# Performance work log

Hardware: AMD Instinct MI355X
Metric: run time of the kernel (lower is better)

Reference implementation:

```python
import jax, jax.numpy as jnp
import numpy as np

N = 20000        # nodes
E = 640000       # edges (avg degree 32)
IN, H1, H2 = 512, 256, 128

def setup_inputs() -> dict:
    key = jax.random.key(0)
    k_feat, k_ew, k_src, k_dst, k_w1, k_w2 = jax.random.split(key, 6)
    return {
        "features": jax.random.normal(k_feat, (N, IN), jnp.float32),
        "edge_weight": jax.random.uniform(k_ew, (E,), jnp.float32),
        "src": jax.random.randint(k_src, (E,), 0, N),
        "dst": jax.random.randint(k_dst, (E,), 0, N),
        # learned params (GraphConv weight uses xavier-style init; bias zeros)
        "W1": jax.random.normal(k_w1, (IN, H1), jnp.float32) / np.float32(np.sqrt(IN)),
        "b1": jnp.zeros((H1,), jnp.float32),
        "W2": jax.random.normal(k_w2, (H1, H2), jnp.float32) / np.float32(np.sqrt(H1)),
        "b2": jnp.zeros((H2,), jnp.float32),
    }

def reference(features, edge_weight, src, dst, W1, b1, W2, b2):
    seg = lambda v, idx: jax.ops.segment_sum(v, idx, num_segments=N)

    # --- EdgeWeightNorm(norm='both'):
    # w_e / sqrt(out_wsum(src_e) * in_wsum(dst_e))
    out_wsum = seg(edge_weight, src)           # weighted out-degree  [N]
    in_wsum = seg(edge_weight, dst)            # weighted in-degree   [N]
    nw = edge_weight * jax.lax.rsqrt(out_wsum[src]) * jax.lax.rsqrt(in_wsum[dst])  # [E]

    # --- GraphConv layer 1: norm='none', edge_weight=nw, relu
    # in_feats > out_feats -> transform first, then weighted aggregation
    h = features @ W1                          # [N, H1]
    h = seg(h[src] * nw[:, None], dst) + b1    # SpMM: sum_e nw_e * h[src_e] at dst
    h = jax.nn.relu(h)

    # --- GraphConv layer 2: norm='both' (plain degrees, clamped min 1), identity act
    ones_e = jnp.ones((E,), h.dtype)
    out_deg = jnp.maximum(seg(ones_e, src), 1.0)   # out-degrees [N]
    in_deg = jnp.maximum(seg(ones_e, dst), 1.0)    # in-degrees  [N]
    h = h * jax.lax.rsqrt(out_deg)[:, None]        # src-side norm
    h = h @ W2                                     # [N, H2] (in > out -> W first)
    h = seg(h[src], dst)                           # unweighted sum aggregation
    h = h * jax.lax.rsqrt(in_deg)[:, None] + b2    # dst-side norm + bias
    return h
```

## Files before the change

kernel.cpp:

```cpp
#include <hip/hip_runtime.h>
#include <hip/hip_bf16.h>
#include <hip/hip_fp16.h>
#include <stdint.h>

#define IN_F 512
#define H1_F 256
#define H2_F 128
#define MPAD 20096
#define NN   20000
#define NPAIR 10000
#define BH   128
#define CAP  128

typedef __attribute__((ext_vector_type(8))) _Float16 half8;
typedef __attribute__((ext_vector_type(4))) float f32x4;
typedef __attribute__((ext_vector_type(4))) uint32_t u32x4;

__device__ inline __half2 h2cast(uint32_t v) { return __builtin_bit_cast(__half2, v); }
__device__ inline uint32_t h2bits(__half2 v) { return __builtin_bit_cast(uint32_t, v); }

__device__ inline void gld_lds16(const uint32_t* g, uint32_t* l) {
    __builtin_amdgcn_global_load_lds((const __attribute__((address_space(1))) uint32_t*)g,
                                     (__attribute__((address_space(3))) uint32_t*)l,
                                     16, 0, 0);
}

__global__ __launch_bounds__(512) void build_and_pack(
        const int* __restrict__ dst, const int* __restrict__ src,
        const float* __restrict__ ew,
        uint32_t* __restrict__ Pd, uint32_t* __restrict__ Ps, int E, int CH,
        const float4* __restrict__ X, ushort4* __restrict__ P, int n4,
        const float* __restrict__ W1, const float* __restrict__ W2,
        uint16_t* __restrict__ Bt1, uint16_t* __restrict__ Bt2) {
    __shared__ uint32_t pd[NN];
    __shared__ uint32_t ps[NN];
    const int b = blockIdx.x, tid = threadIdx.x;
    if (b < BH) {
        for (int i = tid; i < NN; i += 512) { pd[i] = 0; ps[i] = 0; }
        __syncthreads();
        const int e0 = b * CH, e1 = min(e0 + CH, E);
        for (int e = e0 + tid; e < e1; e += 512) {
            uint32_t v = (1u << 24) | (uint32_t)__float2uint_rn(ew[e] * 65536.0f);
            atomicAdd(&pd[dst[e]], v);
            atomicAdd(&ps[src[e]], v);
        }
        __syncthreads();
        for (int i = tid; i < NN; i += 512) {
            Pd[(size_t)b * NN + i] = pd[i];
            Ps[(size_t)b * NN + i] = ps[i];
        }
    } else {
        const int pbid = b - BH;
        const int PBLK = gridDim.x - BH;
        const int stride = PBLK * 512;
        const int t1 = IN_F * H1_F;
        const int total = n4 + t1 + H1_F * H2_F;
        for (int idx = pbid * 512 + tid; idx < total; idx += stride) {
            if (idx < n4) {
                float4 x = X[idx];
                ushort4 o;
                o.x = __builtin_bit_cast(unsigned short, (_Float16)x.x);
                o.y = __builtin_bit_cast(unsigned short, (_Float16)x.y);
                o.z = __builtin_bit_cast(unsigned short, (_Float16)x.z);
                o.w = __builtin_bit_cast(unsigned short, (_Float16)x.w);
                P[idx] = o;
            } else {
                int i = idx - n4;
                if (i < t1) {
                    int k = i / H1_F, n = i - k * H1_F;
                    Bt1[(size_t)n * IN_F + k] =
                        __builtin_bit_cast(unsigned short, (_Float16)W1[i]);
                } else {
                    int i2 = i - t1;
                    int k = i2 / H2_F, n = i2 - k * H2_F;
                    Bt2[(size_t)n * H1_F + k] =
                        __builtin_bit_cast(unsigned short, (_Float16)W2[i2]);
                }
            }
        }
    }
}

__global__ void offsets_kernel(const uint32_t* __restrict__ Pd,
                               const uint32_t* __restrict__ Ps,
                               uint16_t* __restrict__ Od,
                               int* __restrict__ in_cnt, int* __restrict__ out_cnt,
                               float* __restrict__ in_rs, float* __restrict__ out_rs, int N) {
    int i = blockIdx.x * blockDim.x + threadIdx.x;
    if (i >= N) return;
    uint32_t cin = 0, cout = 0, win = 0, wout = 0;
    for (int b = 0; b < BH; ++b) {
        uint32_t vd = Pd[(size_t)b * NN + i];
        Od[(size_t)b * NN + i] = (uint16_t)cin;
        cin += vd >> 24; win += vd & 0xFFFFFFu;
        uint32_t vs = Ps[(size_t)b * NN + i];
        cout += vs >> 24; wout += vs & 0xFFFFFFu;
    }
    in_cnt[i] = (int)cin;
    out_cnt[i] = (int)cout;
    in_rs[i]  = cin  ? rsqrtf((float)win  * (1.0f / 65536.0f)) : 0.f;
    out_rs[i] = cout ? rsqrtf((float)wout * (1.0f / 65536.0f)) : 0.f;
}

__global__ __launch_bounds__(512) void scatter_dst(
        const int* __restrict__ src, const int* __restrict__ dst,
        const float* __restrict__ ew,
        const uint16_t* __restrict__ Od,
        const float* __restrict__ in_rs, const float* __restrict__ out_rs,
        unsigned long long* __restrict__ s_pk, int E, int CH) {
    __shared__ uint32_t h[NPAIR];
    const int b = blockIdx.x, tid = threadIdx.x;
    for (int i = tid; i < NPAIR; i += 512) h[i] = 0;
    __syncthreads();
    const int e0 = b * CH, e1 = min(e0 + CH, E);
    const uint16_t* Ob = Od + (size_t)b * NN;
    for (int e = e0 + tid; e < e1; e += 512) {
        int d = dst[e];
        uint32_t old = atomicAdd(&h[d >> 1], 1u << ((d & 1) * 16));
        uint32_t rank = (old >> ((d & 1) * 16)) & 0xffffu;
        int s = src[e];
        float nw = ew[e] * out_rs[s] * in_rs[d];
        int p = d * CAP + (int)Ob[d] + (int)rank;
        s_pk[p] = (unsigned long long)(unsigned)s |
                  ((unsigned long long)__builtin_bit_cast(unsigned, nw) << 32);
    }
}

template <bool ROWSCALE>
__global__ __launch_bounds__(256, 1) void gemm_f16(
        const uint16_t* __restrict__ At, const uint16_t* __restrict__ Bt,
        __half* __restrict__ Cout, const int* __restrict__ rowcnt,
        int M, int Nout, int K) {
    __shared__ uint32_t Al[128 * 16];
    __shared__ uint32_t Bl[128 * 16];
    const int tid = threadIdx.x;
    const int lane = tid & 63, wid = tid >> 6;
    const int wm = wid >> 1, wn = wid & 1;
    const int l15 = lane & 15, lhi = lane >> 4;
    const int brow = blockIdx.x * 128, bcol = blockIdx.y * 128;

    f32x4 acc[4][4];
#pragma unroll
    for (int m = 0; m < 4; ++m)
#pragma unroll
        for (int n = 0; n < 4; ++n) acc[m][n] = f32x4{0.f, 0.f, 0.f, 0.f};

    for (int k0 = 0; k0 < K; k0 += 32) {
#pragma unroll
        for (int i = 0; i < 2; ++i) {
            int chunk = i * 256 + tid;
            int r = chunk >> 2, c16 = chunk & 3;
            int c16s = c16 ^ ((r & 3) ^ ((r >> 2) & 3));
            gld_lds16((const uint32_t*)(At + (size_t)(brow + r) * K + k0) + c16s * 4,
                      Al + chunk * 4);
        }
#pragma unroll
        for (int i = 0; i < 2; ++i) {
            int chunk = i * 256 + tid;
            int r = chunk >> 2, c16 = chunk & 3;
            int c16s = c16 ^ ((r & 3) ^ ((r >> 2) & 3));
            gld_lds16((const uint32_t*)(Bt + (size_t)(bcol + r) * K + k0) + c16s * 4,
                      Bl + chunk * 4);
        }
        __syncthreads();

        half8 am[4], bm[4];
#pragma unroll
        for (int m = 0; m < 4; ++m) {
            int row = wm * 64 + m * 16 + l15;
            int sA = (row & 3) ^ ((row >> 2) & 3);
            am[m] = __builtin_bit_cast(half8,
                        *(const u32x4*)(Al + row * 16 + ((lhi ^ sA) << 2)));
        }
#pragma unroll
        for (int n = 0; n < 4; ++n) {
            int col = wn * 64 + n * 16 + l15;
            int sB = (col & 3) ^ ((col >> 2) & 3);
            bm[n] = __builtin_bit_cast(half8,
                        *(const u32x4*)(Bl + col * 16 + ((lhi ^ sB) << 2)));
        }

#pragma unroll
        for (int m = 0; m < 4; ++m)
#pragma unroll
            for (int n = 0; n < 4; ++n)
                acc[m][n] = __builtin_amdgcn_mfma_f32_16x16x32_f16(am[m], bm[n],
                                                                   acc[m][n], 0, 0, 0);
        __syncthreads();
    }

#pragma unroll
    for (int m = 0; m < 4; ++m) {
        int rbase = brow + wm * 64 + m * 16 + lhi * 4;
        float scl[4];
#pragma unroll
        for (int j = 0; j < 4; ++j) {
            scl[j] = 1.f;
            if (ROWSCALE && rbase + j < M)
                scl[j] = rsqrtf(fmaxf((float)rowcnt[rbase + j], 1.f));
        }
#pragma unroll
        for (int n = 0; n < 4; ++n) {
            int col = bcol + wn * 64 + n * 16 + l15;
#pragma unroll
            for (int j = 0; j < 4; ++j) {
                int row = rbase + j;
                if (row < M)
                    Cout[(size_t)row * Nout + col] = __float2half(acc[m][n][j] * scl[j]);
            }
        }
    }
}

__global__ void spmm1_h2(const uint4* __restrict__ h4,
                         const unsigned long long* __restrict__ s_pk,
                         const int* __restrict__ in_cnt,
                         const float* __restrict__ b1, uint16_t* __restrict__ h1f, int N) {
    int bx = blockIdx.x;
    int slice = bx & 3;
    int grp = bx >> 2;
    int wid = threadIdx.x >> 6, lane = threadIdx.x & 63;
    int node = grp * 4 + wid;
    if (node >= N) return;
    int start = node * CAP, cnt = in_cnt[node];
    int s_pre = 0; uint32_t w2_pre = 0;
    if (lane < cnt) {
        unsigned long long m = s_pk[start + lane];
        s_pre = (int)(unsigned)m;
        __half hw = __float2half(__builtin_bit_cast(float, (unsigned)(m >> 32)));
        w2_pre = h2bits(__halves2half2(hw, hw));
    }
    int el = lane >> 3, fo = lane & 7;
    const uint4* hb = h4 + slice * 8 + fo;
    __half2 acc[4];
#pragma unroll
    for (int k = 0; k < 4; ++k) acc[k] = h2cast(0u);
    int cnt1 = min(cnt, 64);
    int nb = (cnt1 + 7) >> 3;
    int s[8]; uint32_t w[8]; uint4 v[8];
#pragma unroll
    for (int g = 0; g < 8; ++g) {
        if (g < nb) {
            int j = el + g * 8;
            s[g] = __shfl(s_pre, j);
            w[g] = (uint32_t)__shfl((int)w2_pre, j);
            v[g] = hb[(size_t)s[g] * 32];
        }
    }
#pragma unroll
    for (int g = 0; g < 8; ++g) {
        if (g < nb) {
            __half2 wg = h2cast(w[g]);
            acc[0] = __hfma2(wg, h2cast(v[g].x), acc[0]);
            acc[1] = __hfma2(wg, h2cast(v[g].y), acc[1]);
            acc[2] = __hfma2(wg, h2cast(v[g].z), acc[2]);
            acc[3] = __hfma2(wg, h2cast(v[g].w), acc[3]);
        }
    }
    for (int j = 64 + el; j < cnt; j += 8) {
        unsigned long long m = s_pk[start + j];
        int sx = (int)(unsigned)m;
        __half hw = __float2half(__builtin_bit_cast(float, (unsigned)(m >> 32)));
        __half2 w2h = __halves2half2(hw, hw);
        uint4 vx = hb[(size_t)sx * 32];
        acc[0] = __hfma2(w2h, h2cast(vx.x), acc[0]);
        acc[1] = __hfma2(w2h, h2cast(vx.y), acc[1]);
        acc[2] = __hfma2(w2h, h2cast(vx.z), acc[2]);
        acc[3] = __hfma2(w2h, h2cast(vx.w), acc[3]);
    }
#pragma unroll
    for (int d = 8; d < 64; d <<= 1)
#pragma unroll
        for (int k = 0; k < 4; ++k) {
            uint32_t o = (uint32_t)__shfl_xor((int)h2bits(acc[k]), d);
            acc[k] = __hadd2(acc[k], h2cast(o));
        }
    if (el == 0) {
        int fi = slice * 64 + fo * 8;
        float2 f0 = __half22float2(acc[0]);
        float2 f1 = __half22float2(acc[1]);
        float2 f2 = __half22float2(acc[2]);
        float2 f3 = __half22float2(acc[3]);
        uint4 o;
        o.x = h2bits(__halves2half2(__float2half(fmaxf(f0.x + b1[fi + 0], 0.f)),
                                    __float2half(fmaxf(f0.y + b1[fi + 1], 0.f))));
        o.y = h2bits(__halves2half2(__float2half(fmaxf(f1.x + b1[fi + 2], 0.f)),
                                    __float2half(fmaxf(f1.y + b1[fi + 3], 0.f))));
        o.z = h2bits(__halves2half2(__float2half(fmaxf(f2.x + b1[fi + 4], 0.f)),
                                    __float2half(fmaxf(f2.y + b1[fi + 5], 0.f))));
        o.w = h2bits(__halves2half2(__float2half(fmaxf(f3.x + b1[fi + 6], 0.f)),
                                    __float2half(fmaxf(f3.y + b1[fi + 7], 0.f))));
        *(uint4*)(h1f + (size_t)node * H1_F + fi) = o;
    }
}

__global__ void spmm2_h2(const uint4* __restrict__ h4,
                         const unsigned long long* __restrict__ s_pk,
                         const int* __restrict__ in_cnt,
                         const float* __restrict__ b2, float* __restrict__ out, int N) {
    const uint32_t ONE2 = 0x3C003C00u;
    int bx = blockIdx.x;
    int slice = bx & 1;
    int grp = bx >> 1;
    int wid = threadIdx.x >> 6, lane = threadIdx.x & 63;
    int node = grp * 4 + wid;
    if (node >= N) return;
    int start = node * CAP, cnt = in_cnt[node];
    int s_pre = 0;
    if (lane < cnt) s_pre = (int)(unsigned)s_pk[start + lane];
    int el = lane >> 3, fo = lane & 7;
    const uint4* hb = h4 + slice * 8 + fo;
    __half2 acc0[4], acc1[4];
#pragma unroll
    for (int k = 0; k < 4; ++k) { acc0[k] = h2cast(0u); acc1[k] = h2cast(0u); }
    int cnt1 = min(cnt, 64);
    int nb = (cnt1 + 7) >> 3;
    int s[8]; __half2 w[8]; uint4 v[8];
#pragma unroll
    for (int g = 0; g < 8; ++g) {
        if (g < nb) {
            int j = el + g * 8;
            s[g] = __shfl(s_pre, j);
            w[g] = h2cast((j < cnt1) ? ONE2 : 0u);
            v[g] = hb[(size_t)s[g] * 16];
        }
    }
#pragma unroll
    for (int g = 0; g < 4; ++g) {
        if (g < nb) {
            acc0[0] = __hfma2(w[g], h2cast(v[g].x), acc0[0]);
            acc0[1] = __hfma2(w[g], h2cast(v[g].y), acc0[1]);
            acc0[2] = __hfma2(w[g], h2cast(v[g].z), acc0[2]);
            acc0[3] = __hfma2(w[g], h2cast(v[g].w), acc0[3]);
        }
    }
#pragma unroll
    for (int g = 4; g < 8; ++g) {
        if (g < nb) {
            acc1[0] = __hfma2(w[g], h2cast(v[g].x), acc1[0]);
            acc1[1] = __hfma2(w[g], h2cast(v[g].y), acc1[1]);
            acc1[2] = __hfma2(w[g], h2cast(v[g].z), acc1[2]);
            acc1[3] = __hfma2(w[g], h2cast(v[g].w), acc1[3]);
        }
    }
    for (int j = 64 + el; j < cnt; j += 8) {
        int sx = (int)(unsigned)s_pk[start + j];
        uint4 vx = hb[(size_t)sx * 16];
        __half2 one = h2cast(ONE2);
        acc0[0] = __hfma2(one, h2cast(vx.x), acc0[0]);
        acc0[1] = __hfma2(one, h2cast(vx.y), acc0[1]);
        acc0[2] = __hfma2(one, h2cast(vx.z), acc0[2]);
        acc0[3] = __hfma2(one, h2cast(vx.w), acc0[3]);
    }
    float accf[8];
#pragma unroll
    for (int k = 0; k < 4; ++k) {
        float2 a = __half22float2(acc0[k]);
        float2 b = __half22float2(acc1[k]);
        accf[2 * k]     = a.x + b.x;
        accf[2 * k + 1] = a.y + b.y;
    }
#pragma unroll
    for (int d = 8; d < 64; d <<= 1)
#pragma unroll
        for (int k = 0; k < 8; ++k) accf[k] += __shfl_xor(accf[k], d);
    if (el == 0) {
        float rin = rsqrtf(fmaxf((float)cnt, 1.f));
        int fi = slice * 64 + fo * 8;
        f32x4 r0, r1;
        r0.x = accf[0] * rin + b2[fi + 0];
        r0.y = accf[1] * rin + b2[fi + 1];
        r0.z = accf[2] * rin + b2[fi + 2];
        r0.w = accf[3] * rin + b2[fi + 3];
        r1.x = accf[4] * rin + b2[fi + 4];
        r1.y = accf[5] * rin + b2[fi + 5];
        r1.z = accf[6] * rin + b2[fi + 6];
        r1.w = accf[7] * rin + b2[fi + 7];
        float* dp = out + (size_t)node * H2_F + fi;
        *(f32x4*)dp = r0;
        *(f32x4*)(dp + 4) = r1;
    }
}

extern "C" void kernel_launch(void* const* d_in, const int* in_sizes, int n_in,
                              void* d_out, int out_size, void* d_ws, size_t ws_size,
                              hipStream_t stream) {
    const float* features = (const float*)d_in[0];
    const float* edge_w   = (const float*)d_in[1];
    const int*   src      = (const int*)d_in[2];
    const int*   dst      = (const int*)d_in[3];
    const float* W1       = (const float*)d_in[4];
    const float* b1       = (const float*)d_in[5];
    const float* W2       = (const float*)d_in[6];
    const float* b2       = (const float*)d_in[7];
    float* out = (float*)d_out;

    const int N = in_sizes[0] / IN_F;
    const int E = in_sizes[1];
    const int CH = (E + BH - 1) / BH;

    char* base = (char*)d_ws;
    size_t off = 0;
    auto alloc = [&](size_t bytes) {
        char* p = base + off;
        off = (off + bytes + 255) & ~(size_t)255;
        return p;
    };
    int*   out_cnt   = (int*)  alloc((size_t)N * 4);
    float* out_rs    = (float*)alloc((size_t)N * 4);
    int*   in_cnt    = (int*)  alloc((size_t)N * 4);
    float* in_rs     = (float*)alloc((size_t)N * 4);
    unsigned long long* s_pk = (unsigned long long*)alloc((size_t)NN * CAP * 8);
    uint16_t* Bt1    = (uint16_t*)alloc((size_t)H1_F * IN_F * 2);
    uint16_t* Bt2    = (uint16_t*)alloc((size_t)H2_F * H1_F * 2);
    __half* h_f16    = (__half*)alloc((size_t)MPAD * H1_F * 2);
    uint16_t* feat16 = (uint16_t*)alloc((size_t)MPAD * IN_F * 2);
    uint32_t* big    = (uint32_t*)alloc((size_t)BH * NN * 4 * 2 + (size_t)BH * NN * 2);
    uint32_t* Pd = big;
    uint32_t* Ps = big + (size_t)BH * NN;
    uint16_t* Od = (uint16_t*)(Ps + (size_t)BH * NN);
    uint16_t* h1f = (uint16_t*)big;
    __half*   h2f = (__half*)((uint16_t*)big + (size_t)MPAD * H1_F);
    (void)ws_size;

    build_and_pack<<<256, 512, 0, stream>>>(dst, src, edge_w, Pd, Ps, E, CH,
                                            (const float4*)features, (ushort4*)feat16,
                                            N * IN_F / 4, W1, W2, Bt1, Bt2);
    offsets_kernel<<<(N + 255) / 256, 256, 0, stream>>>(Pd, Ps, Od, in_cnt, out_cnt,
                                                        in_rs, out_rs, N);
    scatter_dst<<<BH, 512, 0, stream>>>(src, dst, edge_w, Od,
                                        in_rs, out_rs, s_pk, E, CH);

    dim3 g1(MPAD / 128, H1_F / 128);
    gemm_f16<false><<<g1, 256, 0, stream>>>(feat16, Bt1, h_f16, nullptr, N, H1_F, IN_F);
    int grp = (N + 3) / 4;
    spmm1_h2<<<grp * 4, 256, 0, stream>>>((const uint4*)h_f16, s_pk,
                                          in_cnt, b1, h1f, N);
    dim3 g2(MPAD / 128, 1);
    gemm_f16<true><<<g2, 256, 0, stream>>>(h1f, Bt2, h2f, out_cnt, N, H2_F, H1_F);
    spmm2_h2<<<grp * 2, 256, 0, stream>>>((const uint4*)h2f, s_pk,
                                          in_cnt, b2, out, N);
}
```

Before: 139.9 us.

## Merge layer-1 GEMM and degree-offset scan into one heterogeneous launch

Measured after the change: 127.7 us. 1.1x faster.

```diff
diff --git a/kernel.cpp b/kernel.cpp
--- a/kernel.cpp
+++ b/kernel.cpp
@@ -11,6 +11,7 @@
 #define NPAIR 10000
 #define BH   128
 #define CAP  128
+#define GB1  (157 * 2)
 
 typedef __attribute__((ext_vector_type(8))) _Float16 half8;
 typedef __attribute__((ext_vector_type(4))) float f32x4;
@@ -81,25 +82,104 @@
     }
 }
 
-__global__ void offsets_kernel(const uint32_t* __restrict__ Pd,
-                               const uint32_t* __restrict__ Ps,
-                               uint16_t* __restrict__ Od,
-                               int* __restrict__ in_cnt, int* __restrict__ out_cnt,
-                               float* __restrict__ in_rs, float* __restrict__ out_rs, int N) {
-    int i = blockIdx.x * blockDim.x + threadIdx.x;
-    if (i >= N) return;
-    uint32_t cin = 0, cout = 0, win = 0, wout = 0;
-    for (int b = 0; b < BH; ++b) {
-        uint32_t vd = Pd[(size_t)b * NN + i];
-        Od[(size_t)b * NN + i] = (uint16_t)cin;
-        cin += vd >> 24; win += vd & 0xFFFFFFu;
-        uint32_t vs = Ps[(size_t)b * NN + i];
-        cout += vs >> 24; wout += vs & 0xFFFFFFu;
-    }
-    in_cnt[i] = (int)cin;
-    out_cnt[i] = (int)cout;
-    in_rs[i]  = cin  ? rsqrtf((float)win  * (1.0f / 65536.0f)) : 0.f;
-    out_rs[i] = cout ? rsqrtf((float)wout * (1.0f / 65536.0f)) : 0.f;
+__global__ __launch_bounds__(256, 1) void gemm1_and_offsets(
+        const uint16_t* __restrict__ At, const uint16_t* __restrict__ Bt,
+        __half* __restrict__ Cout, int M, int K,
+        const uint32_t* __restrict__ Pd, const uint32_t* __restrict__ Ps,
+        uint16_t* __restrict__ Od,
+        int* __restrict__ in_cnt, int* __restrict__ out_cnt,
+        float* __restrict__ in_rs, float* __restrict__ out_rs, int N) {
+    __shared__ uint32_t Al[128 * 16];
+    __shared__ uint32_t Bl[128 * 16];
+    const int bx = blockIdx.x;
+    const int tid = threadIdx.x;
+    if (bx >= GB1) {
+        int i = (bx - GB1) * 256 + tid;
+        if (i >= N) return;
+        uint32_t cin = 0, cout = 0, win = 0, wout = 0;
+        for (int b = 0; b < BH; ++b) {
+            uint32_t vd = Pd[(size_t)b * NN + i];
+            Od[(size_t)b * NN + i] = (uint16_t)cin;
+            cin += vd >> 24; win += vd & 0xFFFFFFu;
+            uint32_t vs = Ps[(size_t)b * NN + i];
+            cout += vs >> 24; wout += vs & 0xFFFFFFu;
+        }
+        in_cnt[i] = (int)cin;
+        out_cnt[i] = (int)cout;
+        in_rs[i]  = cin  ? rsqrtf((float)win  * (1.0f / 65536.0f)) : 0.f;
+        out_rs[i] = cout ? rsqrtf((float)wout * (1.0f / 65536.0f)) : 0.f;
+        return;
+    }
+    const int xg = bx % 157, yg = bx / 157;
+    const int lane = tid & 63, wid = tid >> 6;
+    const int wm = wid >> 1, wn = wid & 1;
+    const int l15 = lane & 15, lhi = lane >> 4;
+    const int brow = xg * 128, bcol = yg * 128;
+
+    f32x4 acc[4][4];
+#pragma unroll
+    for (int m = 0; m < 4; ++m)
+#pragma unroll
+        for (int n = 0; n < 4; ++n) acc[m][n] = f32x4{0.f, 0.f, 0.f, 0.f};
+
+    for (int k0 = 0; k0 < K; k0 += 32) {
+#pragma unroll
+        for (int i = 0; i < 2; ++i) {
+            int chunk = i * 256 + tid;
+            int r = chunk >> 2, c16 = chunk & 3;
+            int c16s = c16 ^ ((r & 3) ^ ((r >> 2) & 3));
+            gld_lds16((const uint32_t*)(At + (size_t)(brow + r) * K + k0) + c16s * 4,
+                      Al + chunk * 4);
+        }
+#pragma unroll
+        for (int i = 0; i < 2; ++i) {
+            int chunk = i * 256 + tid;
+            int r = chunk >> 2, c16 = chunk & 3;
+            int c16s = c16 ^ ((r & 3) ^ ((r >> 2) & 3));
+            gld_lds16((const uint32_t*)(Bt + (size_t)(bcol + r) * K + k0) + c16s * 4,
+                      Bl + chunk * 4);
+        }
+        __syncthreads();
+
+        half8 am[4], bm[4];
+#pragma unroll
+        for (int m = 0; m < 4; ++m) {
+            int row = wm * 64 + m * 16 + l15;
+            int sA = (row & 3) ^ ((row >> 2) & 3);
+            am[m] = __builtin_bit_cast(half8,
+                        *(const u32x4*)(Al + row * 16 + ((lhi ^ sA) << 2)));
+        }
+#pragma unroll
+        for (int n = 0; n < 4; ++n) {
+            int col = wn * 64 + n * 16 + l15;
+            int sB = (col & 3) ^ ((col >> 2) & 3);
+            bm[n] = __builtin_bit_cast(half8,
+                        *(const u32x4*)(Bl + col * 16 + ((lhi ^ sB) << 2)));
+        }
+
+#pragma unroll
+        for (int m = 0; m < 4; ++m)
+#pragma unroll
+            for (int n = 0; n < 4; ++n)
+                acc[m][n] = __builtin_amdgcn_mfma_f32_16x16x32_f16(am[m], bm[n],
+                                                                   acc[m][n], 0, 0, 0);
+        __syncthreads();
+    }
+
+#pragma unroll
+    for (int m = 0; m < 4; ++m) {
+        int rbase = brow + wm * 64 + m * 16 + lhi * 4;
+#pragma unroll
+        for (int n = 0; n < 4; ++n) {
+            int col = bcol + wn * 64 + n * 16 + l15;
+#pragma unroll
+            for (int j = 0; j < 4; ++j) {
+                int row = rbase + j;
+                if (row < M)
+                    Cout[(size_t)row * H1_F + col] = __float2half(acc[m][n][j]);
+            }
+        }
+    }
 }
 
 __global__ __launch_bounds__(512) void scatter_dst(
@@ -126,8 +206,7 @@
     }
 }
 
-template <bool ROWSCALE>
-__global__ __launch_bounds__(256, 1) void gemm_f16(
+__global__ __launch_bounds__(256, 1) void gemm2_f16(
         const uint16_t* __restrict__ At, const uint16_t* __restrict__ Bt,
         __half* __restrict__ Cout, const int* __restrict__ rowcnt,
         int M, int Nout, int K) {
@@ -196,7 +275,7 @@
 #pragma unroll
         for (int j = 0; j < 4; ++j) {
             scl[j] = 1.f;
-            if (ROWSCALE && rbase + j < M)
+            if (rbase + j < M)
                 scl[j] = rsqrtf(fmaxf((float)rowcnt[rbase + j], 1.f));
         }
 #pragma unroll
@@ -426,18 +505,20 @@
     build_and_pack<<<256, 512, 0, stream>>>(dst, src, edge_w, Pd, Ps, E, CH,
                                             (const float4*)features, (ushort4*)feat16,
                                             N * IN_F / 4, W1, W2, Bt1, Bt2);
-    offsets_kernel<<<(N + 255) / 256, 256, 0, stream>>>(Pd, Ps, Od, in_cnt, out_cnt,
-                                                        in_rs, out_rs, N);
+
+    int goBlocks = GB1 + (N + 255) / 256;
+    gemm1_and_offsets<<<goBlocks, 256, 0, stream>>>(feat16, Bt1, h_f16, N, IN_F,
+                                                    Pd, Ps, Od, in_cnt, out_cnt,
+                                                    in_rs, out_rs, N);
+
     scatter_dst<<<BH, 512, 0, stream>>>(src, dst, edge_w, Od,
                                         in_rs, out_rs, s_pk, E, CH);
 
-    dim3 g1(MPAD / 128, H1_F / 128);
-    gemm_f16<false><<<g1, 256, 0, stream>>>(feat16, Bt1, h_f16, nullptr, N, H1_F, IN_F);
     int grp = (N + 3) / 4;
     spmm1_h2<<<grp * 4, 256, 0, stream>>>((const uint4*)h_f16, s_pk,
                                           in_cnt, b1, h1f, N);
     dim3 g2(MPAD / 128, 1);
-    gemm_f16<true><<<g2, 256, 0, stream>>>(h1f, Bt2, h2f, out_cnt, N, H2_F, H1_F);
+    gemm2_f16<<<g2, 256, 0, stream>>>(h1f, Bt2, h2f, out_cnt, N, H2_F, H1_F);
     spmm2_h2<<<grp * 2, 256, 0, stream>>>((const uint4*)h2f, s_pk,
                                           in_cnt, b2, out, N);
 }
```
